# Optimization experiments

Measured on AMD Instinct MI355X. Metric: run time of the kernel, lower is better.

Reference implementation:

```python
import jax, jax.numpy as jnp
import numpy as np

D_MODEL = 1024
H = 16
D_K = D_MODEL // H


def setup_inputs() -> dict:
    key = jax.random.key(0)
    ks = jax.random.split(key, 7)
    B, S = 4, 2048
    scale = 1.0 / np.sqrt(D_MODEL)
    return {
        "q": jax.random.normal(ks[0], (B, S, D_MODEL), dtype=jnp.float32),
        "k": jax.random.normal(ks[1], (B, S, D_MODEL), dtype=jnp.float32),
        "v": jax.random.normal(ks[2], (B, S, D_MODEL), dtype=jnp.float32),
        "W_q": jax.random.normal(ks[3], (D_MODEL, D_MODEL), dtype=jnp.float32) * scale,
        "W_k": jax.random.normal(ks[4], (D_MODEL, D_MODEL), dtype=jnp.float32) * scale,
        "W_v": jax.random.normal(ks[5], (D_MODEL, D_MODEL), dtype=jnp.float32) * scale,
        "W_o": jax.random.normal(ks[6], (D_MODEL, D_MODEL), dtype=jnp.float32) * scale,
    }


def reference(q, k, v, W_q, W_k, W_v, W_o):
    B, S, _ = q.shape
    # nn.Linear(bias=False): y = x @ W.T
    def proj(x, W):
        return (x @ W.T).reshape(B, -1, H, D_K).transpose(0, 2, 1, 3)  # [B,H,S,d_k]
    Q = proj(q, W_q)
    K = proj(k, W_k)
    V = proj(v, W_v)
    scores = jnp.einsum('bhqd,bhkd->bhqk', Q, K) / jnp.sqrt(jnp.float32(D_K))
    attn = jax.nn.softmax(scores, axis=-1)  # dropout p=0.0 -> identity
    ctx = jnp.einsum('bhqk,bhkd->bhqd', attn, V)
    ctx = ctx.transpose(0, 2, 1, 3).reshape(B, S, H * D_K)
    return ctx @ W_o.T
```

## Files before the change

kernel.cpp:

```cpp
#include <hip/hip_runtime.h>
#include <stdint.h>


typedef __attribute__((ext_vector_type(8))) short bf16x8;
typedef __attribute__((ext_vector_type(4))) float f32x4;

__device__ __forceinline__ void lds_async16(const void* g, void* l) {
  __builtin_amdgcn_global_load_lds(
      (const __attribute__((address_space(1))) void*)g,
      (__attribute__((address_space(3))) void*)l, 16, 0, 0);
}

__device__ __forceinline__ unsigned short f2bf(float f) {
  union { float f; unsigned u; } v; v.f = f;
  unsigned u = v.u + 0x7fffu + ((v.u >> 16) & 1u);
  return (unsigned short)(u >> 16);
}

__device__ __forceinline__ float fast_exp2(float x) {
#if __has_builtin(__builtin_amdgcn_exp2f)
  return __builtin_amdgcn_exp2f(x);
#else
  return exp2f(x);
#endif
}

__device__ __forceinline__ uint2 pack4(float a, float b, float c, float d) {
#if __has_builtin(__builtin_amdgcn_cvt_pk_bf16_f32)
  typedef __bf16 bf16v2 __attribute__((ext_vector_type(2)));
  union U { bf16v2 v; unsigned u; };
  U x, y;
  x.v = __builtin_amdgcn_cvt_pk_bf16_f32(a, b);
  y.v = __builtin_amdgcn_cvt_pk_bf16_f32(c, d);
  return make_uint2(x.u, y.u);
#else
  return make_uint2((unsigned)f2bf(a) | ((unsigned)f2bf(b) << 16),
                    (unsigned)f2bf(c) | ((unsigned)f2bf(d) << 16));
#endif
}

__global__ void cvt_kernel(const float* s0, const float* s1, const float* s2, const float* s3,
                           unsigned short* d0, unsigned short* d1, unsigned short* d2, unsigned short* d3,
                           int n4) {
  int which = blockIdx.y;
  const float* s = which == 0 ? s0 : which == 1 ? s1 : which == 2 ? s2 : s3;
  unsigned short* d = which == 0 ? d0 : which == 1 ? d1 : which == 2 ? d2 : d3;
  int i = blockIdx.x * 256 + threadIdx.x;
  if (i < n4) {
    float4 v = ((const float4*)s)[i];
    ushort4 o;
    o.x = f2bf(v.x); o.y = f2bf(v.y); o.z = f2bf(v.z); o.w = f2bf(v.w);
    ((ushort4*)d)[i] = o;
  }
}

struct GemmAcc { f32x4 acc[4][4]; };

__device__ __forceinline__ void gemm_core(const unsigned short* __restrict__ Arows,
                                          const unsigned short* __restrict__ Brows,
                                          int tm, int tn, unsigned short* As,
                                          unsigned short* Bs, GemmAcc& g) {
  constexpr int K = 1024;
  const int tid = threadIdx.x;
  const int lane = tid & 63;
  const int wv = tid >> 6;
  const int wm = wv & 1, wn = wv >> 1;
  const int c16 = lane & 15, q4 = lane >> 4;

#pragma unroll
  for (int i = 0; i < 4; ++i)
#pragma unroll
    for (int j = 0; j < 4; ++j)
#pragma unroll
      for (int r = 0; r < 4; ++r) g.acc[i][j][r] = 0.f;

  const int srow = tid >> 3;
  const int gc = (((tid & 7) ^ (srow & 7)) << 3);
  const unsigned short* Arow = Arows + (size_t)(tm * 128 + srow) * K + gc;
  const unsigned short* Brow = Brows + (size_t)(tn * 128 + srow) * K + gc;
  char* AsBase = (char*)As + tid * 16;
  char* BsBase = (char*)Bs + tid * 16;

  for (int k0 = 0; k0 < K; k0 += 64) {
    __syncthreads();
#pragma unroll
    for (int i = 0; i < 4; ++i) {
      lds_async16(Arow + k0 + i * 32 * K, AsBase + i * 4096);
      lds_async16(Brow + k0 + i * 32 * K, BsBase + i * 4096);
    }
    __syncthreads();
#pragma unroll
    for (int ks = 0; ks < 2; ++ks) {
      bf16x8 af[4], bfr[4];
#pragma unroll
      for (int i = 0; i < 4; ++i) {
        int mr = wm * 64 + i * 16 + c16;
        int pa = (ks * 4 + q4) ^ (mr & 7);
        af[i] = *(const bf16x8*)(As + mr * 64 + pa * 8);
        int nr = wn * 64 + i * 16 + c16;
        int pb = (ks * 4 + q4) ^ (nr & 7);
        bfr[i] = *(const bf16x8*)(Bs + nr * 64 + pb * 8);
      }
#pragma unroll
      for (int i = 0; i < 4; ++i)
#pragma unroll
        for (int j = 0; j < 4; ++j)
          g.acc[i][j] = __builtin_amdgcn_mfma_f32_16x16x32_bf16(af[i], bfr[j], g.acc[i][j], 0, 0, 0);
    }
  }
}

__global__ __launch_bounds__(256, 2)
void qkv_kernel(const unsigned short* __restrict__ qb, const unsigned short* __restrict__ kb,
                const unsigned short* __restrict__ vb,
                const unsigned short* __restrict__ wq, const unsigned short* __restrict__ wk,
                const unsigned short* __restrict__ wv_,
                unsigned short* __restrict__ Qb, unsigned short* __restrict__ Kb,
                unsigned short* __restrict__ Vtb) {
  __shared__ unsigned short As[128 * 64];
  __shared__ unsigned short Bs[128 * 64];
  const int z = blockIdx.z;
  const unsigned short* A;
  const unsigned short* B;
  int tm, tn;
  if (z == 0)      { A = qb;  B = wq;  tm = blockIdx.y; tn = blockIdx.x; }
  else if (z == 1) { A = kb;  B = wk;  tm = blockIdx.y; tn = blockIdx.x; }
  else             { A = wv_; B = vb;  tm = blockIdx.x; tn = blockIdx.y; }

  GemmAcc g;
  gemm_core(A, B, tm, tn, As, Bs, g);

  const int lane = threadIdx.x & 63;
  const int wv = threadIdx.x >> 6;
  const int wm = wv & 1, wn = wv >> 1;
  const int c16 = lane & 15, q4 = lane >> 4;
  const float qscale = 0.125f * 1.44269504f;

#pragma unroll
  for (int i = 0; i < 4; ++i)
#pragma unroll
    for (int j = 0; j < 4; ++j)
#pragma unroll
      for (int r = 0; r < 4; ++r) {
        int m = tm * 128 + wm * 64 + i * 16 + q4 * 4 + r;
        int n = tn * 128 + wn * 64 + j * 16 + c16;
        float val = g.acc[i][j][r];
        if (z < 2) {
          if (z == 0) val *= qscale;
          int b = m >> 11, s_ = m & 2047, h = n >> 6, d = n & 63;
          unsigned short* dst = z == 0 ? Qb : Kb;
          dst[(((size_t)(b * 16 + h) * 2048 + s_) << 6) | d] = f2bf(val);
        } else {
          int h = m >> 6, d = m & 63, b = n >> 11, s_ = n & 2047;
          Vtb[((size_t)((b * 16 + h) * 64 + d) << 11) | s_] = f2bf(val);
        }
      }
}

__global__ __launch_bounds__(256, 2)
void out_gemm(const unsigned short* __restrict__ A, const unsigned short* __restrict__ B,
              float* __restrict__ C) {
  __shared__ unsigned short As[128 * 64];
  __shared__ unsigned short Bs[128 * 64];
  GemmAcc g;
  gemm_core(A, B, blockIdx.y, blockIdx.x, As, Bs, g);
  const int lane = threadIdx.x & 63;
  const int wv = threadIdx.x >> 6;
  const int wm = wv & 1, wn = wv >> 1;
  const int c16 = lane & 15, q4 = lane >> 4;
#pragma unroll
  for (int i = 0; i < 4; ++i)
#pragma unroll
    for (int j = 0; j < 4; ++j)
#pragma unroll
      for (int r = 0; r < 4; ++r) {
        int m = blockIdx.y * 128 + wm * 64 + i * 16 + q4 * 4 + r;
        int n = blockIdx.x * 128 + wn * 64 + j * 16 + c16;
        C[(size_t)m * 1024 + n] = g.acc[i][j][r];
      }
}

constexpr int PSS = 72;

__global__ __launch_bounds__(256, 3)
void attn_kernel(const unsigned short* __restrict__ Q,
                 const unsigned short* __restrict__ K,
                 const unsigned short* __restrict__ Vt,
                 unsigned short* __restrict__ ctx) {
  __shared__ unsigned short Ks[2][64 * 64];
  __shared__ unsigned short Vs[2][64 * 64];
  __shared__ unsigned short Ps[128 * PSS];

  const int tid = threadIdx.x, lane = tid & 63, w = tid >> 6;
  const int c16 = lane & 15, q4 = lane >> 4;
  const int wbase = w * 32;

  const int idx = blockIdx.x;
  const int slot = idx >> 3;
  const int bh = (idx & 7) * 8 + (slot >> 4);
  const int qt = slot & 15;

  const unsigned short* Qp = Q + ((size_t)bh * 2048 + qt * 128) * 64;
  const unsigned short* Kp = K + (size_t)bh * 2048 * 64;
  const unsigned short* Vp = Vt + (size_t)bh * 64 * 2048;

  const int srow8 = tid >> 3;
  const int gc8 = (((tid & 7) ^ (srow8 & 7)) << 3);

  const unsigned short* Krs = Kp + (size_t)srow8 * 64 + gc8;
  const unsigned short* Vrs = Vp + (size_t)srow8 * 2048 + gc8;
  char* KdBase = (char*)&Ks[0][0] + tid * 16;
  char* VdBase = (char*)&Vs[0][0] + tid * 16;

  {
    const unsigned short* Qr = Qp + (size_t)srow8 * 64 + gc8;
    char* base = (char*)Ps + tid * 16;
#pragma unroll
    for (int c = 0; c < 4; ++c) lds_async16(Qr + c * 32 * 64, base + c * 4096);
  }
#pragma unroll
  for (int c = 0; c < 2; ++c) {
    lds_async16(Krs + c * 2048, KdBase + c * 4096);
    lds_async16(Vrs + c * 65536, VdBase + c * 4096);
  }
  __syncthreads();

  bf16x8 qf[2][2];
#pragma unroll
  for (int nn = 0; nn < 2; ++nn)
#pragma unroll
    for (int ks = 0; ks < 2; ++ks) {
      int qr = wbase + nn * 16 + c16;
      int pos = (ks * 4 + q4) ^ (qr & 7);
      qf[nn][ks] = *(const bf16x8*)(Ps + qr * 64 + pos * 8);
    }
  __syncthreads();

  bf16x8 onesf;
  {
    short v = (c16 == 0) ? (short)0x3F80 : (short)0;
#pragma unroll
    for (int j = 0; j < 8; ++j) onesf[j] = v;
  }

  f32x4 oacc[2][4];
  f32x4 lacc[2];
#pragma unroll
  for (int mm = 0; mm < 2; ++mm) {
#pragma unroll
    for (int r = 0; r < 4; ++r) lacc[mm][r] = 0.f;
#pragma unroll
    for (int dj = 0; dj < 4; ++dj)
#pragma unroll
      for (int r = 0; r < 4; ++r) oacc[mm][dj][r] = 0.f;
  }

  const int kb0 = c16 * 64 + ((q4 ^ (c16 & 7)) * 8);
  const int kb1 = c16 * 64 + (((4 + q4) ^ (c16 & 7)) * 8);
  int vbo[2];
#pragma unroll
  for (int ks2 = 0; ks2 < 2; ++ks2)
    vbo[ks2] = c16 * 64 + (((ks2 * 4 + q4) ^ (c16 & 7)) * 8);
  const unsigned short* pb0 = Ps + (wbase + c16) * PSS + q4 * 8;
  unsigned short* pw0 = Ps + (wbase + c16) * PSS + q4 * 4;
  unsigned short* pw1 = pw0 + 16 * PSS;

  for (int kt = 0; kt < 32; ++kt) {
    const unsigned short* KsC = &Ks[kt & 1][0];
    const unsigned short* VsC = &Vs[kt & 1][0];
    if (kt < 31) {
      int nb = (kt + 1) & 1;
      size_t ko = (size_t)(kt + 1) * 4096;
      size_t vo = (size_t)(kt + 1) * 64;
#pragma unroll
      for (int c = 0; c < 2; ++c) {
        lds_async16(Krs + ko + c * 2048, KdBase + nb * 8192 + c * 4096);
        lds_async16(Vrs + vo + c * 65536, VdBase + nb * 8192 + c * 4096);
      }
    }

#pragma unroll
    for (int m = 0; m < 4; ++m) {
      bf16x8 kf0 = *(const bf16x8*)(KsC + kb0 + m * 1024);
      bf16x8 kf1 = *(const bf16x8*)(KsC + kb1 + m * 1024);
      f32x4 s0 = {0.f, 0.f, 0.f, 0.f}, s1 = {0.f, 0.f, 0.f, 0.f};
      s0 = __builtin_amdgcn_mfma_f32_16x16x32_bf16(kf0, qf[0][0], s0, 0, 0, 0);
      s0 = __builtin_amdgcn_mfma_f32_16x16x32_bf16(kf1, qf[0][1], s0, 0, 0, 0);
      s1 = __builtin_amdgcn_mfma_f32_16x16x32_bf16(kf0, qf[1][0], s1, 0, 0, 0);
      s1 = __builtin_amdgcn_mfma_f32_16x16x32_bf16(kf1, qf[1][1], s1, 0, 0, 0);
      *(uint2*)(pw0 + m * 16) =
          pack4(fast_exp2(s0[0]), fast_exp2(s0[1]), fast_exp2(s0[2]), fast_exp2(s0[3]));
      *(uint2*)(pw1 + m * 16) =
          pack4(fast_exp2(s1[0]), fast_exp2(s1[1]), fast_exp2(s1[2]), fast_exp2(s1[3]));
    }

#pragma unroll
    for (int ks2 = 0; ks2 < 2; ++ks2) {
      bf16x8 vfr[4];
#pragma unroll
      for (int dj = 0; dj < 4; ++dj) vfr[dj] = *(const bf16x8*)(VsC + vbo[ks2] + dj * 1024);
      bf16x8 pf0 = *(const bf16x8*)(pb0 + ks2 * 32);
      bf16x8 pf1 = *(const bf16x8*)(pb0 + ks2 * 32 + 16 * PSS);
      lacc[0] = __builtin_amdgcn_mfma_f32_16x16x32_bf16(pf0, onesf, lacc[0], 0, 0, 0);
      lacc[1] = __builtin_amdgcn_mfma_f32_16x16x32_bf16(pf1, onesf, lacc[1], 0, 0, 0);
#pragma unroll
      for (int dj = 0; dj < 4; ++dj) {
        oacc[0][dj] = __builtin_amdgcn_mfma_f32_16x16x32_bf16(pf0, vfr[dj], oacc[0][dj], 0, 0, 0);
        oacc[1][dj] = __builtin_amdgcn_mfma_f32_16x16x32_bf16(pf1, vfr[dj], oacc[1][dj], 0, 0, 0);
      }
    }

    __syncthreads();
  }

  int b = bh >> 4, h = bh & 15;
#pragma unroll
  for (int mm = 0; mm < 2; ++mm)
#pragma unroll
    for (int r = 0; r < 4; ++r) {
      float l = __shfl(lacc[mm][r], lane & 48, 64);
      float inv = 1.f / l;
      int s_ = qt * 128 + wbase + mm * 16 + q4 * 4 + r;
#pragma unroll
      for (int dj = 0; dj < 4; ++dj) {
        int d = dj * 16 + c16;
        ctx[((size_t)(b * 2048 + s_)) * 1024 + h * 64 + d] = f2bf(oacc[mm][dj][r] * inv);
      }
    }
}

extern "C" void kernel_launch(void* const* d_in, const int* in_sizes, int n_in,
                              void* d_out, int out_size, void* d_ws, size_t ws_size,
                              hipStream_t stream) {
  const float* q  = (const float*)d_in[0];
  const float* k  = (const float*)d_in[1];
  const float* v  = (const float*)d_in[2];
  const float* Wq = (const float*)d_in[3];
  const float* Wk = (const float*)d_in[4];
  const float* Wv = (const float*)d_in[5];
  const float* Wo = (const float*)d_in[6];

  char* ws = (char*)d_ws;
  unsigned short* qb  = (unsigned short*)(ws);
  unsigned short* kb  = (unsigned short*)(ws + (16u << 20));
  unsigned short* vb  = (unsigned short*)(ws + (32u << 20));
  unsigned short* wqb = (unsigned short*)(ws + (48u << 20));
  unsigned short* wkb = (unsigned short*)(ws + (50u << 20));
  unsigned short* wvb = (unsigned short*)(ws + (52u << 20));
  unsigned short* wob = (unsigned short*)(ws + (54u << 20));
  unsigned short* Qb  = (unsigned short*)(ws + (56u << 20));
  unsigned short* Kb  = (unsigned short*)(ws + (72u << 20));
  unsigned short* Vtb = (unsigned short*)(ws + (88u << 20));
  unsigned short* ctxb = qb;

  cvt_kernel<<<dim3(1024, 4), 256, 0, stream>>>(Wq, Wk, Wv, Wo, wqb, wkb, wvb, wob, 262144);
  cvt_kernel<<<dim3(8192, 3), 256, 0, stream>>>(q, k, v, q, qb, kb, vb, qb, 2097152);

  qkv_kernel<<<dim3(8, 64, 3), 256, 0, stream>>>(qb, kb, vb, wqb, wkb, wvb, Qb, Kb, Vtb);

  attn_kernel<<<dim3(1024), 256, 0, stream>>>(Qb, Kb, Vtb, ctxb);

  out_gemm<<<dim3(8, 64), 256, 0, stream>>>(ctxb, wob, (float*)d_out);
}
```

Baseline: 343.8 us.

## Keep softmax probabilities in registers and feed PV via 16x16x16 MFMA

The attention kernel no longer writes exp'd scores to a shared-memory P buffer and reads them back. The S accumulator layout is reused directly as the A operand of 16x16x16 bf16 MFMAs, with V fragments read in a matching 4-element layout. This removes LDS round-trips for P and the Q-buffer aliasing sync, and frees LDS that may help occupancy. In exchange it issues twice as many, smaller MFMAs (K=16 instead of 32), which have lower throughput per instruction, and uses narrower LDS reads for V.

After: 351.2 us. 2.2% more time.

```diff
diff --git a/kernel.cpp b/kernel.cpp
--- a/kernel.cpp
+++ b/kernel.cpp
@@ -3,6 +3,7 @@
 
 
 typedef __attribute__((ext_vector_type(8))) short bf16x8;
+typedef __attribute__((ext_vector_type(4))) short bf16x4;
 typedef __attribute__((ext_vector_type(4))) float f32x4;
 
 __device__ __forceinline__ void lds_async16(const void* g, void* l) {
@@ -36,6 +37,20 @@
 #else
   return make_uint2((unsigned)f2bf(a) | ((unsigned)f2bf(b) << 16),
                     (unsigned)f2bf(c) | ((unsigned)f2bf(d) << 16));
+#endif
+}
+
+__device__ __forceinline__ bf16x4 pack4b(float a, float b, float c, float d) {
+  union { uint2 u; bf16x4 s; } x;
+  x.u = pack4(a, b, c, d);
+  return x.s;
+}
+
+__device__ __forceinline__ f32x4 mfma16(bf16x4 a, bf16x4 b, f32x4 c) {
+#if __has_builtin(__builtin_amdgcn_mfma_f32_16x16x16_bf16)
+  return __builtin_amdgcn_mfma_f32_16x16x16_bf16(a, b, c, 0, 0, 0);
+#else
+  return __builtin_amdgcn_mfma_f32_16x16x16bf16_1k(a, b, c, 0, 0, 0);
 #endif
 }
 
@@ -180,16 +195,14 @@
       }
 }
 
-constexpr int PSS = 72;
-
 __global__ __launch_bounds__(256, 3)
 void attn_kernel(const unsigned short* __restrict__ Q,
                  const unsigned short* __restrict__ K,
                  const unsigned short* __restrict__ Vt,
                  unsigned short* __restrict__ ctx) {
+  __shared__ unsigned short Qs[128 * 64];
   __shared__ unsigned short Ks[2][64 * 64];
   __shared__ unsigned short Vs[2][64 * 64];
-  __shared__ unsigned short Ps[128 * PSS];
 
   const int tid = threadIdx.x, lane = tid & 63, w = tid >> 6;
   const int c16 = lane & 15, q4 = lane >> 4;
@@ -214,7 +227,7 @@
 
   {
     const unsigned short* Qr = Qp + (size_t)srow8 * 64 + gc8;
-    char* base = (char*)Ps + tid * 16;
+    char* base = (char*)Qs + tid * 16;
 #pragma unroll
     for (int c = 0; c < 4; ++c) lds_async16(Qr + c * 32 * 64, base + c * 4096);
   }
@@ -232,15 +245,14 @@
     for (int ks = 0; ks < 2; ++ks) {
       int qr = wbase + nn * 16 + c16;
       int pos = (ks * 4 + q4) ^ (qr & 7);
-      qf[nn][ks] = *(const bf16x8*)(Ps + qr * 64 + pos * 8);
-    }
-  __syncthreads();
-
-  bf16x8 onesf;
+      qf[nn][ks] = *(const bf16x8*)(Qs + qr * 64 + pos * 8);
+    }
+
+  bf16x4 ones4;
   {
     short v = (c16 == 0) ? (short)0x3F80 : (short)0;
 #pragma unroll
-    for (int j = 0; j < 8; ++j) onesf[j] = v;
+    for (int j = 0; j < 4; ++j) ones4[j] = v;
   }
 
   f32x4 oacc[2][4];
@@ -257,13 +269,10 @@
 
   const int kb0 = c16 * 64 + ((q4 ^ (c16 & 7)) * 8);
   const int kb1 = c16 * 64 + (((4 + q4) ^ (c16 & 7)) * 8);
-  int vbo[2];
-#pragma unroll
-  for (int ks2 = 0; ks2 < 2; ++ks2)
-    vbo[ks2] = c16 * 64 + (((ks2 * 4 + q4) ^ (c16 & 7)) * 8);
-  const unsigned short* pb0 = Ps + (wbase + c16) * PSS + q4 * 8;
-  unsigned short* pw0 = Ps + (wbase + c16) * PSS + q4 * 4;
-  unsigned short* pw1 = pw0 + 16 * PSS;
+  int vb_[4];
+#pragma unroll
+  for (int m = 0; m < 4; ++m)
+    vb_[m] = c16 * 64 + (((m * 2 + (q4 >> 1)) ^ (c16 & 7)) * 8) + (q4 & 1) * 4;
 
   for (int kt = 0; kt < 32; ++kt) {
     const unsigned short* KsC = &Ks[kt & 1][0];
@@ -288,25 +297,18 @@
       s0 = __builtin_amdgcn_mfma_f32_16x16x32_bf16(kf1, qf[0][1], s0, 0, 0, 0);
       s1 = __builtin_amdgcn_mfma_f32_16x16x32_bf16(kf0, qf[1][0], s1, 0, 0, 0);
       s1 = __builtin_amdgcn_mfma_f32_16x16x32_bf16(kf1, qf[1][1], s1, 0, 0, 0);
-      *(uint2*)(pw0 + m * 16) =
-          pack4(fast_exp2(s0[0]), fast_exp2(s0[1]), fast_exp2(s0[2]), fast_exp2(s0[3]));
-      *(uint2*)(pw1 + m * 16) =
-          pack4(fast_exp2(s1[0]), fast_exp2(s1[1]), fast_exp2(s1[2]), fast_exp2(s1[3]));
-    }
-
-#pragma unroll
-    for (int ks2 = 0; ks2 < 2; ++ks2) {
-      bf16x8 vfr[4];
-#pragma unroll
-      for (int dj = 0; dj < 4; ++dj) vfr[dj] = *(const bf16x8*)(VsC + vbo[ks2] + dj * 1024);
-      bf16x8 pf0 = *(const bf16x8*)(pb0 + ks2 * 32);
-      bf16x8 pf1 = *(const bf16x8*)(pb0 + ks2 * 32 + 16 * PSS);
-      lacc[0] = __builtin_amdgcn_mfma_f32_16x16x32_bf16(pf0, onesf, lacc[0], 0, 0, 0);
-      lacc[1] = __builtin_amdgcn_mfma_f32_16x16x32_bf16(pf1, onesf, lacc[1], 0, 0, 0);
+      bf16x4 pf0 = pack4b(fast_exp2(s0[0]), fast_exp2(s0[1]), fast_exp2(s0[2]), fast_exp2(s0[3]));
+      bf16x4 pf1 = pack4b(fast_exp2(s1[0]), fast_exp2(s1[1]), fast_exp2(s1[2]), fast_exp2(s1[3]));
+
+      bf16x4 vfr[4];
+#pragma unroll
+      for (int dj = 0; dj < 4; ++dj) vfr[dj] = *(const bf16x4*)(VsC + vb_[m] + dj * 1024);
+      lacc[0] = mfma16(pf0, ones4, lacc[0]);
+      lacc[1] = mfma16(pf1, ones4, lacc[1]);
 #pragma unroll
       for (int dj = 0; dj < 4; ++dj) {
-        oacc[0][dj] = __builtin_amdgcn_mfma_f32_16x16x32_bf16(pf0, vfr[dj], oacc[0][dj], 0, 0, 0);
-        oacc[1][dj] = __builtin_amdgcn_mfma_f32_16x16x32_bf16(pf1, vfr[dj], oacc[1][dj], 0, 0, 0);
+        oacc[0][dj] = mfma16(pf0, vfr[dj], oacc[0][dj]);
+        oacc[1][dj] = mfma16(pf1, vfr[dj], oacc[1][dj]);
       }
     }
 
```
